# Optimization experiments

Hardware: AMD Instinct MI355X
Metric: run time of the kernel (lower is better)

## Reference

```python
import jax, jax.numpy as jnp
import numpy as np

N = 100_000      # nodes
E = 1_600_000    # edges (avg degree 16)
IN_DIM = 165
HIDDEN = 64
OUT_DIM = 2


def setup_inputs() -> dict:
    key = jax.random.key(0)
    ks = jax.random.split(key, 10)
    x = jax.random.normal(ks[0], (N, IN_DIM), dtype=jnp.float32)
    edge_index = jax.random.randint(ks[1], (2, E), 0, N, dtype=jnp.int32)
    def lin(k, fan_in, fan_out):
        lim = 1.0 / np.sqrt(fan_in)
        return jax.random.uniform(k, (fan_in, fan_out), jnp.float32, -lim, lim)
    # SAGEConv: lin_l (neighbor path, with bias), lin_r (root path, no bias)
    W1l = lin(ks[2], IN_DIM, HIDDEN); b1 = jnp.zeros((HIDDEN,), jnp.float32)
    W1r = lin(ks[3], IN_DIM, HIDDEN)
    W2l = lin(ks[4], HIDDEN, HIDDEN); b2 = jnp.zeros((HIDDEN,), jnp.float32)
    W2r = lin(ks[5], HIDDEN, HIDDEN)
    Wc = lin(ks[6], HIDDEN, OUT_DIM)
    bc = jax.random.uniform(ks[7], (OUT_DIM,), jnp.float32, -0.1, 0.1)
    return {"x": x, "edge_index": edge_index, "W1l": W1l, "b1": b1, "W1r": W1r,
            "W2l": W2l, "b2": b2, "W2r": W2r, "Wc": Wc, "bc": bc}


def _sage_conv(h, src, dst, Wl, bl, Wr):
    # mean-aggregate source features at destination nodes, then two linears
    msg = h[src]                                              # [E, D] gather
    agg = jax.ops.segment_sum(msg, dst, num_segments=N)       # [N, D] scatter-add
    cnt = jax.ops.segment_sum(jnp.ones((src.shape[0], 1), h.dtype), dst,
                              num_segments=N)                 # [N, 1] in-degree
    mean = agg / jnp.maximum(cnt, 1.0)
    return mean @ Wl + bl + h @ Wr


def reference(x, edge_index, W1l, b1, W1r, W2l, b2, W2r, Wc, bc):
    src, dst = edge_index[0], edge_index[1]
    h = jax.nn.relu(_sage_conv(x, src, dst, W1l, b1, W1r))
    # dropout is a no-op at inference (training=False)
    h = jax.nn.relu(_sage_conv(h, src, dst, W2l, b2, W2r))
    return h @ Wc + bc
```

## Files before the change

### kernel.cpp

```cpp
#include <hip/hip_runtime.h>
#include <hip/hip_fp16.h>
#include <cstdint>

#define NN 100000
#define NE 1600000
#define INDIM 165
#define HID 64
#define KP1 192
#define KP2 64

constexpr int BSH = 7;
constexpr int BNODES = 128;
constexpr int NBUK = (NN + BNODES - 1) / BNODES;
constexpr int SC_CHUNK = 8192;
constexpr int BCAP = 2816;

typedef _Float16 f16x8 __attribute__((ext_vector_type(8)));
typedef _Float16 h2 __attribute__((ext_vector_type(2)));
typedef float f32x4 __attribute__((ext_vector_type(4)));

__device__ __forceinline__ void gload16(const float* g, float* l) {
    __builtin_amdgcn_global_load_lds(
        (const __attribute__((address_space(1))) uint32_t*)g,
        (__attribute__((address_space(3))) uint32_t*)l, 16, 0, 0);
}


__global__ __launch_bounds__(256) void k_bscan(const int* __restrict__ bcnt,
                                               int* __restrict__ bbase,
                                               const float* __restrict__ W1l,
                                               const float* __restrict__ W1r,
                                               const float* __restrict__ W2l,
                                               const float* __restrict__ W2r,
                                               _Float16* __restrict__ Wt1,
                                               _Float16* __restrict__ Wt2) {
    if (blockIdx.x > 0) {
        int o = (blockIdx.x - 1) * 256 + threadIdx.x;
        if (o < 128 * KP1) {
            int c = o / KP1, k = o - c * KP1;
            float v = 0.f;
            if (k < INDIM) v = (c < HID) ? W1l[k * HID + c] : W1r[k * HID + (c - HID)];
            Wt1[o] = (_Float16)v;
        } else if (o < 128 * KP1 + 128 * KP2) {
            int p = o - 128 * KP1;
            int c = p / KP2, k = p - c * KP2;
            float v = (c < HID) ? W2l[k * HID + c] : W2r[k * HID + (c - HID)];
            Wt2[p] = (_Float16)v;
        }
        return;
    }
    __shared__ int wsum[4];
    const int tid = threadIdx.x, lane = tid & 63, wid = tid >> 6;
    int v[4];
    int tsum = 0;
#pragma unroll
    for (int i = 0; i < 4; ++i) {
        int idx = tid * 4 + i;
        v[i] = (idx < NBUK) ? bcnt[idx] : 0;
        tsum += v[i];
    }
    int x = tsum;
#pragma unroll
    for (int off = 1; off < 64; off <<= 1) {
        int y = __shfl_up(x, off, 64);
        if (lane >= off) x += y;
    }
    if (lane == 63) wsum[wid] = x;
    __syncthreads();
    int woff = 0;
#pragma unroll
    for (int w = 0; w < 4; ++w)
        if (w < wid) woff += wsum[w];
    int run = woff + x - tsum;
#pragma unroll
    for (int i = 0; i < 4; ++i) {
        int idx = tid * 4 + i;
        if (idx < NBUK) bbase[idx] = run;
        run += v[i];
    }
    if (tid == 255) bbase[NBUK] = woff + x;
}


__global__ __launch_bounds__(256) void k_scatter(const int* __restrict__ src,
                                                 const int* __restrict__ dst,
                                                 int* __restrict__ bcnt,
                                                 unsigned* __restrict__ Eb, int ne) {
    __shared__ int hist[NBUK];
    __shared__ int base[NBUK];
    const int tid = threadIdx.x;
    const int cs = blockIdx.x * SC_CHUNK;
    for (int b = tid; b < NBUK; b += 256) hist[b] = 0;
    __syncthreads();
    unsigned pack[SC_CHUNK / 256];
#pragma unroll 8
    for (int i = 0; i < SC_CHUNK / 256; ++i) {
        int e = cs + i * 256 + tid;
        if (e < ne) {
            int b = dst[e] >> BSH;
            int r = atomicAdd(&hist[b], 1);
            pack[i] = (unsigned)((b << 13) | r);
        } else {
            pack[i] = 0xFFFFFFFFu;
        }
    }
    __syncthreads();
    for (int b = tid; b < NBUK; b += 256) {
        int c = hist[b];
        base[b] = c ? atomicAdd(&bcnt[b], c) : 0;
    }
    __syncthreads();
#pragma unroll 8
    for (int i = 0; i < SC_CHUNK / 256; ++i) {
        if (pack[i] != 0xFFFFFFFFu) {
            int e = cs + i * 256 + tid;
            int b = pack[i] >> 13, r = pack[i] & 8191;
            int pos = base[b] + r;
            if (pos < BCAP)
                Eb[(size_t)b * BCAP + pos] =
                    (unsigned)src[e] | ((unsigned)(dst[e] & (BNODES - 1)) << 17);
        }
    }
}


__global__ __launch_bounds__(256) void k_csrb(const unsigned* __restrict__ Eb,
                                              const int* __restrict__ bbase,
                                              int* __restrict__ rowptr,
                                              int* __restrict__ col, int n) {
    __shared__ int cnt[BNODES];
    __shared__ int pref[BNODES];
    const int tid = threadIdx.x;
    const int gb = bbase[blockIdx.x];
    const int m = bbase[blockIdx.x + 1] - gb;
    const unsigned* eb = Eb + (size_t)blockIdx.x * BCAP;
    for (int i = tid; i < BNODES; i += 256) cnt[i] = 0;
    __syncthreads();
    for (int e = tid; e < m; e += 256)
        atomicAdd(&cnt[eb[e] >> 17], 1);
    __syncthreads();
    if (tid < 64) {
        int c0 = cnt[tid * 2], c1 = cnt[tid * 2 + 1];
        int s = c0 + c1;
        int x = s;
#pragma unroll
        for (int off = 1; off < 64; off <<= 1) {
            int y = __shfl_up(x, off, 64);
            if (tid >= off) x += y;
        }
        int ex = x - s;
        pref[tid * 2] = ex;
        pref[tid * 2 + 1] = ex + c0;
    }
    __syncthreads();
    const int nodeBase = blockIdx.x * BNODES;
    for (int i = tid; i < BNODES; i += 256) {
        int gn = nodeBase + i;
        if (gn < n) rowptr[gn] = gb + pref[i];
        cnt[i] = 0;
    }
    __syncthreads();
    for (int e = tid; e < m; e += 256) {
        unsigned v = eb[e];
        int d = (int)(v >> 17);
        int r = atomicAdd(&cnt[d], 1);
        col[gb + pref[d] + r] = (int)(v & 0x1FFFFu);
    }
    if (blockIdx.x == 0 && tid == 0) rowptr[n] = bbase[NBUK];
}


__global__ __launch_bounds__(256) void k_lin1(const float* __restrict__ X,
                                              const _Float16* __restrict__ Wt,
                                              _Float16* __restrict__ Y,
                                              _Float16* __restrict__ Rh, int n) {
    constexpr int WROWD = 16 * INDIM;
    __shared__ float Xs[4 * WROWD];
    const int tid = threadIdx.x;
    const int lane = tid & 63;
    const int wi = tid >> 6;
    const int jn = lane & 15;
    const int kq = lane >> 4;
    const int r0 = blockIdx.x * 64;
    const int vr = (n - r0 < 64) ? (n - r0) : 64;
    const int cnt = vr * INDIM;
    const float* __restrict__ P = X + (size_t)r0 * INDIM;

    const int myS = wi * WROWD;
    int d = cnt - myS;
    if (d > WROWD) d = WROWD;
    if (d > 0) {
        const int nd = d >> 8;
        for (int i = 0; i < nd; ++i)
            gload16(P + myS + i * 256 + lane * 4, Xs + myS + i * 256);
        for (int i = myS + (nd << 8) + lane; i < myS + d; i += 64)
            Xs[i] = P[i];
        asm volatile("s_waitcnt vmcnt(0)" ::: "memory");
        __builtin_amdgcn_sched_barrier(0);
    }

    const float* xrow = &Xs[(wi * 16 + jn) * INDIM + kq * 8];
    const _Float16* wp = Wt + (size_t)jn * KP1 + kq * 8;

    f32x4 acc[8];
#pragma unroll
    for (int t = 0; t < 8; ++t) acc[t] = (f32x4){0.f, 0.f, 0.f, 0.f};

#pragma unroll
    for (int c = 0; c < 6; ++c) {
        f16x8 xb;
        if (c < 5) {
#pragma unroll
            for (int j = 0; j < 8; ++j) xb[j] = (_Float16)xrow[c * 32 + j];
        } else {
#pragma unroll
            for (int j = 0; j < 8; ++j)
                xb[j] = (kq == 0 && j < 5) ? (_Float16)xrow[160 + j] : (_Float16)0.f;
        }
#pragma unroll
        for (int t = 0; t < 8; ++t) {
            const f16x8 wa = *(const f16x8*)(wp + t * (16 * KP1) + c * 32);
            acc[t] = __builtin_amdgcn_mfma_f32_16x16x32_f16(wa, xb, acc[t], 0, 0, 0);
        }
    }

    const int gn0 = r0 + wi * 16 + jn;
    if (gn0 < n) {
#pragma unroll
        for (int t = 0; t < 8; ++t) {
            const int cb = (t & 3) * 16 + kq * 4;
            union { _Float16 h[4]; uint2 u; } u;
#pragma unroll
            for (int r = 0; r < 4; ++r) u.h[r] = (_Float16)acc[t][r];
            _Float16* dstp = (t < 4) ? (Y + (size_t)gn0 * HID + cb)
                                     : (Rh + (size_t)gn0 * HID + cb);
            *(uint2*)dstp = u.u;
        }
    }
}


template <int KPAD>
__global__ __launch_bounds__(256, 4) void k_linear(const _Float16* __restrict__ Xh,
                                                   const _Float16* __restrict__ Wt,
                                                   _Float16* __restrict__ Y,
                                                   _Float16* __restrict__ Rh, int n) {
    const int tid = threadIdx.x;
    const int lane = tid & 63;
    const int w = tid >> 6;
    const int jn = lane & 15;
    const int kq = lane >> 4;
    const int gn0 = blockIdx.x * 64 + w * 16 + jn;
    const int gn = (gn0 < n) ? gn0 : (n - 1);

    const _Float16* xp = Xh + (size_t)gn * KPAD + kq * 8;
    const _Float16* wp = Wt + (size_t)jn * KPAD + kq * 8;

    f16x8 xf[KPAD / 32];
#pragma unroll
    for (int c = 0; c < KPAD / 32; ++c)
        xf[c] = *(const f16x8*)(xp + c * 32);

    f32x4 acc[8];
#pragma unroll
    for (int t = 0; t < 8; ++t) acc[t] = (f32x4){0.f, 0.f, 0.f, 0.f};

#pragma unroll
    for (int c = 0; c < KPAD / 32; ++c) {
#pragma unroll
        for (int t = 0; t < 8; ++t) {
            const f16x8 wa = *(const f16x8*)(wp + t * (16 * KPAD) + c * 32);
            acc[t] = __builtin_amdgcn_mfma_f32_16x16x32_f16(wa, xf[c], acc[t], 0, 0, 0);
        }
    }

    if (gn0 < n) {
#pragma unroll
        for (int t = 0; t < 8; ++t) {
            const int cb = (t & 3) * 16 + kq * 4;
            union { _Float16 h[4]; uint2 u; } u;
#pragma unroll
            for (int r = 0; r < 4; ++r) u.h[r] = (_Float16)acc[t][r];
            _Float16* dstp = (t < 4) ? (Y + (size_t)gn * HID + cb)
                                     : (Rh + (size_t)gn * HID + cb);
            *(uint2*)dstp = u.u;
        }
    }
}


template <bool CLS>
__global__ __launch_bounds__(256) void k_agg(const _Float16* __restrict__ Y,
                                             const _Float16* __restrict__ Rm,
                                             const float* __restrict__ bias,
                                             const int* __restrict__ rowptr,
                                             const int* __restrict__ col,
                                             _Float16* __restrict__ H,
                                             const float* __restrict__ Wc,
                                             const float* __restrict__ bc,
                                             float* __restrict__ out, int n) {
    const int lane = threadIdx.x & 63;
    const int node = blockIdx.x * 4 + (threadIdx.x >> 6);
    if (node >= n) return;
    const int half_ = lane >> 5;
    const unsigned fp = (unsigned)(lane & 31);
    const h2* __restrict__ Y2 = (const h2*)Y;
    const int s = rowptr[node], e = rowptr[node + 1];
    float ax0 = 0.f, ay0 = 0.f, ax1 = 0.f, ay1 = 0.f;
    int i = s + half_;
    for (; i + 14 < e; i += 16) {
        int c[8];
#pragma unroll
        for (int j = 0; j < 8; ++j) c[j] = col[i + 2 * j];
        h2 y[8];
#pragma unroll
        for (int j = 0; j < 8; ++j) y[j] = Y2[(unsigned)c[j] * 32u + fp];
        h2 b0 = (y[0] + y[1]) + (y[2] + y[3]);
        h2 b1 = (y[4] + y[5]) + (y[6] + y[7]);
        ax0 += (float)b0[0]; ay0 += (float)b0[1];
        ax1 += (float)b1[0]; ay1 += (float)b1[1];
    }
    for (; i + 6 < e; i += 8) {
        int c[4];
#pragma unroll
        for (int j = 0; j < 4; ++j) c[j] = col[i + 2 * j];
        h2 y[4];
#pragma unroll
        for (int j = 0; j < 4; ++j) y[j] = Y2[(unsigned)c[j] * 32u + fp];
        h2 b0 = (y[0] + y[1]) + (y[2] + y[3]);
        ax0 += (float)b0[0]; ay0 += (float)b0[1];
    }
    for (; i < e; i += 2) {
        h2 v = Y2[(unsigned)col[i] * 32u + fp];
        ax0 += (float)v[0]; ay0 += (float)v[1];
    }
    float ax = ax0 + ax1, ay = ay0 + ay1;
    ax += __shfl_xor(ax, 32, 64);
    ay += __shfl_xor(ay, 32, 64);
    const float vx = __shfl(ax, lane >> 1, 64);
    const float vy = __shfl(ay, lane >> 1, 64);
    const float acc = (lane & 1) ? vy : vx;
    const int deg = e - s;
    float h = acc / (float)(deg > 1 ? deg : 1) + bias[lane] +
              (float)Rm[(size_t)node * HID + lane];
    h = fmaxf(h, 0.f);
    if (!CLS) {
        H[(size_t)node * HID + lane] = (_Float16)h;
    } else {
        float p0 = h * Wc[lane * 2 + 0];
        float p1 = h * Wc[lane * 2 + 1];
#pragma unroll
        for (int off = 32; off > 0; off >>= 1) {
            p0 += __shfl_xor(p0, off, 64);
            p1 += __shfl_xor(p1, off, 64);
        }
        if (lane == 0) {
            out[(size_t)node * 2 + 0] = p0 + bc[0];
            out[(size_t)node * 2 + 1] = p1 + bc[1];
        }
    }
}


extern "C" void kernel_launch(void* const* d_in, const int* in_sizes, int n_in,
                              void* d_out, int out_size, void* d_ws, size_t ws_size,
                              hipStream_t stream) {
    const float* x   = (const float*)d_in[0];
    const int*   ei  = (const int*)d_in[1];
    const float* W1l = (const float*)d_in[2];
    const float* b1  = (const float*)d_in[3];
    const float* W1r = (const float*)d_in[4];
    const float* W2l = (const float*)d_in[5];
    const float* b2  = (const float*)d_in[6];
    const float* W2r = (const float*)d_in[7];
    const float* Wc  = (const float*)d_in[8];
    const float* bc  = (const float*)d_in[9];
    float* out = (float*)d_out;
    const int* src = ei;
    const int* dst = ei + NE;

    char* base = (char*)d_ws;
    size_t off = 0;
    auto alloc = [&](size_t bytes) {
        void* p = base + off;
        off = (off + bytes + 255) & ~(size_t)255;
        return p;
    };
    int*      bcnt    = (int*)alloc((size_t)NBUK * 4);
    int*      bbase   = (int*)alloc((size_t)(NBUK + 1) * 4);
    int*      rowptr  = (int*)alloc((size_t)(NN + 1) * 4);
    int*      col     = (int*)alloc((size_t)NE * 4);
    _Float16* Y       = (_Float16*)alloc((size_t)NN * HID * 2 + 256);
    _Float16* Rh      = (_Float16*)alloc((size_t)NN * HID * 2);
    _Float16* Hh      = (_Float16*)alloc((size_t)NN * HID * 2);
    _Float16* Wt1     = (_Float16*)alloc((size_t)128 * KP1 * 2);
    _Float16* Wt2     = (_Float16*)alloc((size_t)128 * KP2 * 2);
    unsigned* Eb      = (unsigned*)Y;

    const int sb = (NE + SC_CHUNK - 1) / SC_CHUNK;
    const int wb = 1 + (128 * KP1 + 128 * KP2 + 255) / 256;

    hipMemsetAsync(bcnt, 0, (size_t)NBUK * 4, stream);
    k_scatter<<<sb, 256, 0, stream>>>(src, dst, bcnt, Eb, NE);
    k_bscan<<<wb, 256, 0, stream>>>(bcnt, bbase, W1l, W1r, W2l, W2r, Wt1, Wt2);
    k_csrb<<<NBUK, 256, 0, stream>>>(Eb, bbase, rowptr, col, NN);

    k_lin1<<<(NN + 63) / 64, 256, 0, stream>>>(x, Wt1, Y, Rh, NN);
    k_agg<false><<<(NN + 3) / 4, 256, 0, stream>>>(Y, Rh, b1, rowptr, col, Hh,
                                                   nullptr, nullptr, nullptr, NN);
    k_linear<KP2><<<(NN + 63) / 64, 256, 0, stream>>>(Hh, Wt2, Y, Rh, NN);
    k_agg<true><<<(NN + 3) / 4, 256, 0, stream>>>(Y, Rh, b2, rowptr, col, nullptr,
                                                  Wc, bc, out, NN);
}
```

Before: 324.7 us.

## Shrink scatter chunks, single-pass CSR build, prefetch first weight slice

The scatter kernel's per-block edge chunk shrinks so more blocks run, with full unrolling of the per-thread loops. The CSR bucket kernel now keeps each edge's value and its atomic rank in registers from the counting pass. That drops the second global read and the second round of shared atomics. The first layer's GEMM issues its first weight-fragment loads before waiting on the async X-to-LDS copy, overlapping the two latencies. Costs: more blocks and more global atomics on bucket counters in scatter, a fixed 11-slot register array that assumes at most 2816 edges per bucket, and the sched_barrier being removed.

```diff
diff --git a/kernel.cpp b/kernel.cpp
--- a/kernel.cpp
+++ b/kernel.cpp
@@ -12,7 +12,7 @@
 constexpr int BSH = 7;
 constexpr int BNODES = 128;
 constexpr int NBUK = (NN + BNODES - 1) / BNODES;
-constexpr int SC_CHUNK = 8192;
+constexpr int SC_CHUNK = 2048;
 constexpr int BCAP = 2816;
 
 typedef _Float16 f16x8 __attribute__((ext_vector_type(8)));
@@ -93,7 +93,7 @@
     for (int b = tid; b < NBUK; b += 256) hist[b] = 0;
     __syncthreads();
     unsigned pack[SC_CHUNK / 256];
-#pragma unroll 8
+#pragma unroll
     for (int i = 0; i < SC_CHUNK / 256; ++i) {
         int e = cs + i * 256 + tid;
         if (e < ne) {
@@ -110,7 +110,7 @@
         base[b] = c ? atomicAdd(&bcnt[b], c) : 0;
     }
     __syncthreads();
-#pragma unroll 8
+#pragma unroll
     for (int i = 0; i < SC_CHUNK / 256; ++i) {
         if (pack[i] != 0xFFFFFFFFu) {
             int e = cs + i * 256 + tid;
@@ -136,8 +136,17 @@
     const unsigned* eb = Eb + (size_t)blockIdx.x * BCAP;
     for (int i = tid; i < BNODES; i += 256) cnt[i] = 0;
     __syncthreads();
-    for (int e = tid; e < m; e += 256)
-        atomicAdd(&cnt[eb[e] >> 17], 1);
+    unsigned ev[11];
+    unsigned short rk[11];
+#pragma unroll
+    for (int j = 0; j < 11; ++j) {
+        int e = tid + j * 256;
+        if (e < m) {
+            unsigned v = eb[e];
+            ev[j] = v;
+            rk[j] = (unsigned short)atomicAdd(&cnt[v >> 17], 1);
+        }
+    }
     __syncthreads();
     if (tid < 64) {
         int c0 = cnt[tid * 2], c1 = cnt[tid * 2 + 1];
@@ -157,14 +166,12 @@
     for (int i = tid; i < BNODES; i += 256) {
         int gn = nodeBase + i;
         if (gn < n) rowptr[gn] = gb + pref[i];
-        cnt[i] = 0;
-    }
-    __syncthreads();
-    for (int e = tid; e < m; e += 256) {
-        unsigned v = eb[e];
-        int d = (int)(v >> 17);
-        int r = atomicAdd(&cnt[d], 1);
-        col[gb + pref[d] + r] = (int)(v & 0x1FFFFu);
+    }
+#pragma unroll
+    for (int j = 0; j < 11; ++j) {
+        int e = tid + j * 256;
+        if (e < m)
+            col[gb + pref[ev[j] >> 17] + rk[j]] = (int)(ev[j] & 0x1FFFFu);
     }
     if (blockIdx.x == 0 && tid == 0) rowptr[n] = bbase[NBUK];
 }
@@ -185,6 +192,7 @@
     const int vr = (n - r0 < 64) ? (n - r0) : 64;
     const int cnt = vr * INDIM;
     const float* __restrict__ P = X + (size_t)r0 * INDIM;
+    const _Float16* wp = Wt + (size_t)jn * KP1 + kq * 8;
 
     const int myS = wi * WROWD;
     int d = cnt - myS;
@@ -195,12 +203,14 @@
             gload16(P + myS + i * 256 + lane * 4, Xs + myS + i * 256);
         for (int i = myS + (nd << 8) + lane; i < myS + d; i += 64)
             Xs[i] = P[i];
-        asm volatile("s_waitcnt vmcnt(0)" ::: "memory");
-        __builtin_amdgcn_sched_barrier(0);
-    }
+    }
+    f16x8 wa0[8];
+#pragma unroll
+    for (int t = 0; t < 8; ++t)
+        wa0[t] = *(const f16x8*)(wp + t * (16 * KP1));
+    asm volatile("s_waitcnt vmcnt(0)" ::: "memory");
 
     const float* xrow = &Xs[(wi * 16 + jn) * INDIM + kq * 8];
-    const _Float16* wp = Wt + (size_t)jn * KP1 + kq * 8;
 
     f32x4 acc[8];
 #pragma unroll
@@ -219,7 +229,8 @@
         }
 #pragma unroll
         for (int t = 0; t < 8; ++t) {
-            const f16x8 wa = *(const f16x8*)(wp + t * (16 * KP1) + c * 32);
+            const f16x8 wa = (c == 0) ? wa0[t]
+                           : *(const f16x8*)(wp + t * (16 * KP1) + c * 32);
             acc[t] = __builtin_amdgcn_mfma_f32_16x16x32_f16(wa, xb, acc[t], 0, 0, 0);
         }
     }
```

Result: no change. 329.7 us (+1.5%).
